# Optimization experiments

Measured on AMD Instinct MI355X. Metric: run time of the kernel, lower is better.

## Reference

```python
import jax, jax.numpy as jnp
import numpy as np

HIDDEN, N_HEADS, N_KV, HD = 2560, 32, 8, 80
B, S = 2, 2048

def apply_rope(x, cos_f, sin_f):
    # x: [B, S, H, hd]; cos_f/sin_f: [S, hd]
    seq_len = x.shape[1]
    cos = cos_f[:seq_len][None, :, None, :]
    sin = sin_f[:seq_len][None, :, None, :]
    hd = x.shape[-1]
    x1, x2 = x[..., : hd // 2], x[..., hd // 2 :]
    return x * cos + jnp.concatenate([-x2, x1], axis=-1) * sin


def setup_inputs() -> dict:
    key = jax.random.key(0)
    ks = jax.random.split(key, 7)
    sd = 0.02
    return {
        "x": jax.random.normal(ks[0], (B, S, HIDDEN), dtype=jnp.float32),
        "cos_f": jax.random.uniform(ks[1], (S, HD), dtype=jnp.float32),
        "sin_f": jax.random.uniform(ks[2], (S, HD), dtype=jnp.float32),
        "Wq": jax.random.normal(ks[3], (HIDDEN, N_HEADS * HD), dtype=jnp.float32) * sd,
        "Wk": jax.random.normal(ks[4], (HIDDEN, N_KV * HD), dtype=jnp.float32) * sd,
        "Wv": jax.random.normal(ks[5], (HIDDEN, N_KV * HD), dtype=jnp.float32) * sd,
        "Wo": jax.random.normal(ks[6], (N_HEADS * HD, HIDDEN), dtype=jnp.float32) * sd,
    }


def reference(x, cos_f, sin_f, Wq, Wk, Wv, Wo):
    b, s, _ = x.shape
    q = (x @ Wq).reshape(b, s, N_HEADS, HD)
    k = (x @ Wk).reshape(b, s, N_KV, HD)
    v = (x @ Wv).reshape(b, s, N_KV, HD)
    q = apply_rope(q, cos_f, sin_f)
    k = apply_rope(k, cos_f, sin_f)
    g = N_HEADS // N_KV
    k = jnp.repeat(k, g, axis=2)  # [b, s, n_heads, hd]
    v = jnp.repeat(v, g, axis=2)
    q, k, v = [jnp.transpose(t, (0, 2, 1, 3)) for t in (q, k, v)]  # [b, h, s, hd]
    scale = jnp.sqrt(jnp.float32(HD))
    w = jnp.einsum("bhqd,bhkd->bhqk", q, k) / scale
    causal = jnp.triu(jnp.full((s, s), -1e9, dtype=w.dtype), k=1)
    w = w + causal[None, None]
    w = jax.nn.softmax(w.astype(jnp.float32), axis=-1).astype(q.dtype)
    o = jnp.einsum("bhqk,bhkd->bhqd", w, v)
    o = jnp.transpose(o, (0, 2, 1, 3)).reshape(b, s, N_HEADS * HD)
    return o @ Wo
```

## Files before the change

kernel.cpp:

```cpp
#include <hip/hip_runtime.h>
#include <hip/hip_bf16.h>
#include <math.h>

#define HIDDEN 2560
#define NH 32
#define NKV 8
#define HD 80
#define BATCH 2
#define SEQ 2048
#define QH_COLS (NH*HD)
#define KV_COLS (NKV*HD)
#define QKV_COLS (QH_COLS + 2*KV_COLS)
#define ROWS (BATCH*SEQ)

typedef __attribute__((ext_vector_type(4))) float floatx4;
typedef __attribute__((ext_vector_type(16))) float floatx16;
typedef __attribute__((ext_vector_type(8))) short shortx8;
typedef __attribute__((ext_vector_type(4))) unsigned short u16x4;
typedef unsigned short u16;

__device__ inline u16 f2bf(float f) { __hip_bfloat16 h = __float2bfloat16(f); return *(u16*)&h; }
__device__ inline void storeC(float v, float* p) { *p = v; }
__device__ inline void storeC(float v, u16* p) { *p = f2bf(v); }

#if __has_builtin(__builtin_amdgcn_exp2f)
__device__ inline float fexp2(float x) { return __builtin_amdgcn_exp2f(x); }
#else
__device__ inline float fexp2(float x) { return __expf(x * 0.6931471805599453f); }
#endif

__device__ __forceinline__ unsigned cvtpk(float lo, float hi2) {
    unsigned r;
    asm("v_cvt_pk_bf16_f32 %0, %1, %2" : "=v"(r) : "v"(lo), "v"(hi2));
    return r;
}
__device__ __forceinline__ void pl32swap(unsigned &a, unsigned &b) {
#if __has_builtin(__builtin_amdgcn_permlane32_swap)
    auto r = __builtin_amdgcn_permlane32_swap(a, b, false, false);
    a = r[0]; b = r[1];
#else
    asm("v_permlane32_swap_b32 %0, %1" : "+v"(a), "+v"(b));
#endif
}

#define GLL(gp, lp) __builtin_amdgcn_global_load_lds( \
    (const __attribute__((address_space(1))) unsigned int*)(gp), \
    (__attribute__((address_space(3))) unsigned int*)(lp), 16, 0, 0)

__global__ __launch_bounds__(256) void conv_bf16(const float* __restrict__ x,
                                                 u16* __restrict__ y) {
    int i = (blockIdx.x * 256 + threadIdx.x) * 4;
    float4 v = *(const float4*)(x + i);
    u16x4 o = { f2bf(v.x), f2bf(v.y), f2bf(v.z), f2bf(v.w) };
    *(u16x4*)(y + i) = o;
}

__global__ __launch_bounds__(256) void transpose_conv(const float* __restrict__ W,
                                                      u16* __restrict__ Wt,
                                                      int K, int N) {
    __shared__ float tile[64][65];
    const int tid = threadIdx.x;
    const int n0 = blockIdx.x * 64, k0 = blockIdx.y * 64;
    const int r = tid >> 4, c4 = (tid & 15) * 4;
#pragma unroll
    for (int i = 0; i < 4; i++) {
        float4 v = *(const float4*)(W + (size_t)(k0 + r + i * 16) * N + n0 + c4);
        tile[r + i * 16][c4 + 0] = v.x;
        tile[r + i * 16][c4 + 1] = v.y;
        tile[r + i * 16][c4 + 2] = v.z;
        tile[r + i * 16][c4 + 3] = v.w;
    }
    __syncthreads();
    const int n = tid >> 2, kg = (tid & 3) * 16;
    __align__(16) u16 tmp[16];
#pragma unroll
    for (int j = 0; j < 16; j++) tmp[j] = f2bf(tile[kg + j][n]);
    u16* dst = Wt + (size_t)(n0 + n) * K + k0 + kg;
    *(uint4*)dst = *(const uint4*)tmp;
    *(uint4*)(dst + 8) = *(const uint4*)(tmp + 8);
}

template <typename OutT>
__global__ __launch_bounds__(512, 2) void gemm256(const u16* __restrict__ A,
                                                  const u16* __restrict__ Bt,
                                                  OutT* __restrict__ C,
                                                  int M, int N, int K) {
    __shared__ __align__(16) u16 SM[65536];
    const int tid = threadIdx.x;
    const int wave = tid >> 6, lane = tid & 63;
    const int m16 = lane & 15, quad = lane >> 4;
    const int wm = wave >> 2, wn = wave & 3;
    const int bm = blockIdx.y * 256, bn = blockIdx.x * 256;

    const int srow = (wave & 3) * 64 + lane;
    const int skc  = wave >> 2;
    const u16* pA = A  + (size_t)(bm + srow) * K + skc * 8;
    const u16* pB = Bt + (size_t)(bn + srow) * K + skc * 8;
    u16* lsA = SM + skc * 2048 + (wave & 3) * 512 + lane * 8;
    u16* lsB = lsA + 32768;

    const int aoff = quad * 2048 + (wm * 128 + m16) * 8;
    const int boff = quad * 2048 + (wn * 64 + m16) * 8 + 32768;

    floatx4 acc[8][4];
#pragma unroll
    for (int i = 0; i < 8; i++)
#pragma unroll
        for (int j = 0; j < 4; j++) acc[i][j] = (floatx4){0.f, 0.f, 0.f, 0.f};

    const int nkt = K >> 6;

#pragma unroll
    for (int t = 0; t < 2; t++) {
        const int tb = t * 16384, tc = t * 64;
        GLL(pA + tc,      lsA + tb);        GLL(pA + tc + 16, lsA + tb + 4096);
        GLL(pB + tc,      lsB + tb);        GLL(pB + tc + 16, lsB + tb + 4096);
        GLL(pA + tc + 32, lsA + tb + 8192); GLL(pA + tc + 48, lsA + tb + 12288);
        GLL(pB + tc + 32, lsB + tb + 8192); GLL(pB + tc + 48, lsB + tb + 12288);
    }
    asm volatile("s_waitcnt vmcnt(8)" ::: "memory");
    __builtin_amdgcn_s_barrier();

    for (int kt = 0; kt < nkt; ++kt) {
        const int ab = (kt & 1) * 16384;
        const bool pf = (kt + 2 < nkt);
        const int pc = (kt + 2) * 64;
        shortx8 af[8], b0, b1, b2, b3;

#pragma unroll
        for (int i = 0; i < 8; i++) af[i] = *(const shortx8*)(SM + ab + aoff + i * 128);
        b0 = *(const shortx8*)(SM + ab + boff);
        b1 = *(const shortx8*)(SM + ab + boff + 128);
        if (pf) { GLL(pA + pc, lsA + ab); GLL(pA + pc + 16, lsA + ab + 4096); }
        __builtin_amdgcn_s_barrier();
        __builtin_amdgcn_s_setprio(1);
#pragma unroll
        for (int i = 0; i < 8; i++) {
            acc[i][0] = __builtin_amdgcn_mfma_f32_16x16x32_bf16(af[i], b0, acc[i][0], 0, 0, 0);
            acc[i][1] = __builtin_amdgcn_mfma_f32_16x16x32_bf16(af[i], b1, acc[i][1], 0, 0, 0);
        }
        __builtin_amdgcn_s_setprio(0);
        __builtin_amdgcn_s_barrier();

        b2 = *(const shortx8*)(SM + ab + boff + 256);
        b3 = *(const shortx8*)(SM + ab + boff + 384);
        if (pf) { GLL(pB + pc, lsB + ab); GLL(pB + pc + 16, lsB + ab + 4096); }
        __builtin_amdgcn_s_barrier();
        __builtin_amdgcn_s_setprio(1);
#pragma unroll
        for (int i = 0; i < 8; i++) {
            acc[i][2] = __builtin_amdgcn_mfma_f32_16x16x32_bf16(af[i], b2, acc[i][2], 0, 0, 0);
            acc[i][3] = __builtin_amdgcn_mfma_f32_16x16x32_bf16(af[i], b3, acc[i][3], 0, 0, 0);
        }
        __builtin_amdgcn_s_setprio(0);
        __builtin_amdgcn_s_barrier();

#pragma unroll
        for (int i = 0; i < 8; i++) af[i] = *(const shortx8*)(SM + ab + 8192 + aoff + i * 128);
        b0 = *(const shortx8*)(SM + ab + 8192 + boff);
        b1 = *(const shortx8*)(SM + ab + 8192 + boff + 128);
        if (pf) { GLL(pA + pc + 32, lsA + ab + 8192); GLL(pA + pc + 48, lsA + ab + 12288); }
        __builtin_amdgcn_s_barrier();
        __builtin_amdgcn_s_setprio(1);
#pragma unroll
        for (int i = 0; i < 8; i++) {
            acc[i][0] = __builtin_amdgcn_mfma_f32_16x16x32_bf16(af[i], b0, acc[i][0], 0, 0, 0);
            acc[i][1] = __builtin_amdgcn_mfma_f32_16x16x32_bf16(af[i], b1, acc[i][1], 0, 0, 0);
        }
        __builtin_amdgcn_s_setprio(0);
        __builtin_amdgcn_s_barrier();

        b2 = *(const shortx8*)(SM + ab + 8192 + boff + 256);
        b3 = *(const shortx8*)(SM + ab + 8192 + boff + 384);
        if (pf) { GLL(pB + pc + 32, lsB + ab + 8192); GLL(pB + pc + 48, lsB + ab + 12288); }
        __builtin_amdgcn_s_barrier();
        __builtin_amdgcn_s_setprio(1);
#pragma unroll
        for (int i = 0; i < 8; i++) {
            acc[i][2] = __builtin_amdgcn_mfma_f32_16x16x32_bf16(af[i], b2, acc[i][2], 0, 0, 0);
            acc[i][3] = __builtin_amdgcn_mfma_f32_16x16x32_bf16(af[i], b3, acc[i][3], 0, 0, 0);
        }
        __builtin_amdgcn_s_setprio(0);
        if (pf) asm volatile("s_waitcnt vmcnt(8)" ::: "memory");
        else    asm volatile("s_waitcnt vmcnt(0)" ::: "memory");
        __builtin_amdgcn_s_barrier();
    }

#pragma unroll
    for (int i = 0; i < 8; i++)
#pragma unroll
        for (int j = 0; j < 4; j++)
#pragma unroll
            for (int p = 0; p < 4; p++) {
                int row = bm + wm * 128 + i * 16 + quad * 4 + p;
                int col = bn + wn * 64 + j * 16 + m16;
                storeC(acc[i][j][p], &C[(size_t)row * N + col]);
            }
}

__global__ __launch_bounds__(256) void rope_bf16(__hip_bfloat16* __restrict__ qkv,
                                                 const float* __restrict__ cf,
                                                 const float* __restrict__ sf) {
    int idx = blockIdx.x * 256 + threadIdx.x;
    int d  = idx % 40;
    int t  = idx / 40;
    int hh = t % (NH + NKV);
    int g  = t / (NH + NKV);
    int s  = g & (SEQ - 1);
    float c1 = cf[s * HD + d],      s1 = sf[s * HD + d];
    float c2 = cf[s * HD + d + 40], s2 = sf[s * HD + d + 40];
    const float qsc = (hh < NH) ? (float)(0.11180339887498949 * 1.4426950408889634) : 1.0f;
    __hip_bfloat16* p = (hh < NH) ? (qkv + (size_t)g * QKV_COLS + hh * HD)
                                  : (qkv + (size_t)g * QKV_COLS + QH_COLS + (hh - NH) * HD);
    float x1 = __bfloat162float(p[d]);
    float x2 = __bfloat162float(p[d + 40]);
    p[d]      = __float2bfloat16((x1 * c1 - x2 * s1) * qsc);
    p[d + 40] = __float2bfloat16((x2 * c2 + x1 * s2) * qsc);
}

__device__ __forceinline__ void stage_K(const u16* kg, u16* dst, int wave, int lane) {
#pragma unroll
    for (int t = 0; t < 2; t++) {
        int s = t * 256 + wave * 64 + lane;
        int db = t * 4 + wave;
        GLL(kg + (size_t)lane * QKV_COLS + db * 8, dst + s * 8);
    }
    if (wave < 2) {
        int s = 512 + wave * 64 + lane;
        int db = 8 + wave;
        GLL(kg + (size_t)lane * QKV_COLS + db * 8, dst + s * 8);
    }
}

__device__ __forceinline__ void load_V(const u16* vg, shortx8* vr, int wave, int lane) {
#pragma unroll
    for (int t = 0; t < 2; t++) {
        int db = t * 4 + wave;
        vr[t] = *(const shortx8*)(vg + (size_t)lane * QKV_COLS + db * 8);
    }
    if (wave < 2) vr[2] = *(const shortx8*)(vg + (size_t)lane * QKV_COLS + (8 + wave) * 8);
}

__device__ __forceinline__ void scatter_V(u16* Vs, const shortx8* vr, int wave, int lane) {
    const int kc = lane >> 3, jj = lane & 7;
    u16* base = Vs + kc * 768 + jj;
#pragma unroll
    for (int t = 0; t < 2; t++) {
        int db = t * 4 + wave;
#pragma unroll
        for (int i = 0; i < 8; i++) base[db * 64 + ((i ^ kc) << 3)] = vr[t][i];
    }
    if (wave < 2) {
        int db = 8 + wave;
#pragma unroll
        for (int i = 0; i < 8; i++) base[db * 64 + ((i ^ kc) << 3)] = vr[2][i];
    }
}

__global__ __launch_bounds__(256, 3) void attn_mfma(const u16* __restrict__ qkv,
                                                    u16* __restrict__ ob) {
    __shared__ __align__(16) u16 SM[16384];
    u16* Kbuf = SM;
    u16* Vs   = SM + 10240;

    const int tid  = threadIdx.x;
    const int wave = tid >> 6;
    const int lane = tid & 63;
    const int l31  = lane & 31;
    const int hi   = lane >> 5;

    const int idx = blockIdx.x;
    const int qt  = 15 - (idx >> 6);
    const int hb  = idx & 63;
    const int h   = hb >> 1;
    const int b   = hb & 1;
    const int kvh = h >> 2;
    const int qb  = qt * 128 + wave * 32;

    const u16* qgb = qkv + (size_t)(b * SEQ + qt * 128) * QKV_COLS + h * HD;
    const u16* kg0 = qkv + (size_t)(b * SEQ) * QKV_COLS + QH_COLS + kvh * HD;
    const u16* vg0 = qkv + (size_t)(b * SEQ) * QKV_COLS + QH_COLS + KV_COLS + kvh * HD;

    {
        int kc = tid >> 5, o = (tid & 31) * 4;
        *(u16x4*)(Vs + kc * 768 + 640 + o) = (u16x4){0, 0, 0, 0};
    }

#pragma unroll
    for (int t = 0; t < 5; t++) {
        int s = t * 256 + tid;
        int row = s / 10, ch = s % 10;
        GLL(qgb + (size_t)row * QKV_COLS + ch * 8, SM + s * 8);
    }
    __syncthreads();
    shortx8 qf[5];
    {
        const u16* qrow = SM + (wave * 32 + l31) * 80 + hi * 8;
#pragma unroll
        for (int c = 0; c < 5; c++) qf[c] = *(const shortx8*)(qrow + c * 16);
    }
    __syncthreads();

    int vbase[4];
#pragma unroll
    for (int c = 0; c < 4; c++) {
        int k8 = c * 2 + hi;
        vbase[c] = k8 * 768 + ((l31 & 24) + ((l31 & 7) ^ k8)) * 8;
    }
    const u16* kfp = Kbuf + hi * 512 + l31 * 8;

    stage_K(kg0, Kbuf, wave, lane);
    shortx8 vr[3];
    load_V(vg0, vr, wave, lane);
    __syncthreads();
    scatter_V(Vs, vr, wave, lane);
    __syncthreads();

    floatx16 Oacc[3];
#pragma unroll
    for (int n = 0; n < 3; n++)
#pragma unroll
        for (int r = 0; r < 16; r++) Oacc[n][r] = 0.0f;
    float mrow = -1.0e30f, lrow = 0.0f;
    int cur = 0;
    const int nkt = 2 * qt + 2;

    for (int kt = 0; kt < nkt; kt++) {
        const bool last = (kt == nkt - 1);
        if (!last) {
            const u16* kg = kg0 + (size_t)(kt + 1) * 64 * QKV_COLS;
            const u16* vg = vg0 + (size_t)(kt + 1) * 64 * QKV_COLS;
            stage_K(kg, Kbuf + (cur ^ 1) * 5120, wave, lane);
            load_V(vg, vr, wave, lane);
        }

        const bool active = (kt * 64 <= qb + 31);
        if (active) {
            const u16* kp = kfp + cur * 5120;
            const bool kr1   = (kt * 64 + 32 <= qb + 31);
            const bool dmask = (kt * 64 + 63 > qb);
            floatx16 S0, S1;
            {
                floatx16 s;
#pragma unroll
                for (int r = 0; r < 16; r++) s[r] = 0.0f;
#pragma unroll
                for (int c = 0; c < 5; c++) {
                    shortx8 kf = *(const shortx8*)(kp + c * 1024);
                    s = __builtin_amdgcn_mfma_f32_32x32x16_bf16(kf, qf[c], s, 0, 0, 0);
                }
                S0 = s;
            }
            if (kr1) {
                floatx16 s;
#pragma unroll
                for (int r = 0; r < 16; r++) s[r] = 0.0f;
#pragma unroll
                for (int c = 0; c < 5; c++) {
                    shortx8 kf = *(const shortx8*)(kp + c * 1024 + 256);
                    s = __builtin_amdgcn_mfma_f32_32x32x16_bf16(kf, qf[c], s, 0, 0, 0);
                }
                S1 = s;
            }
            const int qrel = qb + l31 - kt * 64;
            if (dmask) {
#pragma unroll
                for (int r = 0; r < 16; r++) {
                    int rr = (r & 3) + 8 * (r >> 2) + 4 * hi;
                    if (rr > qrel) S0[r] = -1.0e30f;
                    if (kr1 && (32 + rr) > qrel) S1[r] = -1.0e30f;
                }
            }
            float mx = mrow;
#pragma unroll
            for (int r = 0; r < 16; r++) mx = fmaxf(mx, S0[r]);
            if (kr1) {
#pragma unroll
                for (int r = 0; r < 16; r++) mx = fmaxf(mx, S1[r]);
            }
            mx = fmaxf(mx, __shfl_xor(mx, 32));
            if (!__all(mx - mrow <= 8.0f)) {
                float alpha = fexp2(mrow - mx);
                lrow *= alpha;
#pragma unroll
                for (int n = 0; n < 3; n++)
#pragma unroll
                    for (int r = 0; r < 16; r++) Oacc[n][r] *= alpha;
                mrow = mx;
            }
            float rsum = 0.0f;
#pragma unroll
            for (int r = 0; r < 16; r++) { float p = fexp2(S0[r] - mrow); rsum += p; S0[r] = p; }
            if (kr1) {
#pragma unroll
                for (int r = 0; r < 16; r++) { float p = fexp2(S1[r] - mrow); rsum += p; S1[r] = p; }
            }
            rsum += __shfl_xor(rsum, 32);
            lrow += rsum;

#pragma unroll
            for (int kr = 0; kr < 2; kr++) {
                if (kr == 1 && !kr1) break;
                floatx16& Sv = (kr == 0) ? S0 : S1;
                unsigned d0[4], d1[4];
#pragma unroll
                for (int m = 0; m < 4; m++) {
                    d0[m] = cvtpk(Sv[4 * m + 0], Sv[4 * m + 1]);
                    d1[m] = cvtpk(Sv[4 * m + 2], Sv[4 * m + 3]);
                }
#pragma unroll
                for (int cb = 0; cb < 2; cb++) {
                    int c = kr * 2 + cb;
                    if (kt * 64 + c * 16 > qb + 31) break;
                    unsigned x0 = d0[2 * cb], y0 = d0[2 * cb + 1];
                    unsigned x1 = d1[2 * cb], y1 = d1[2 * cb + 1];
                    pl32swap(x0, y0);
                    pl32swap(x1, y1);
                    union { unsigned u[4]; shortx8 s8; } pf;
                    pf.u[0] = x0; pf.u[1] = x1; pf.u[2] = y0; pf.u[3] = y1;
#pragma unroll
                    for (int n = 0; n < 3; n++) {
                        shortx8 vf = *(const shortx8*)(Vs + vbase[c] + n * 256);
                        Oacc[n] = __builtin_amdgcn_mfma_f32_32x32x16_bf16(vf, pf.s8, Oacc[n], 0, 0, 0);
                    }
                }
            }
        }

        if (last) break;
        __syncthreads();
        scatter_V(Vs, vr, wave, lane);
        cur ^= 1;
        __syncthreads();
    }

    const float invl = 1.0f / lrow;
    u16* op = ob + (size_t)(b * SEQ + qt * 128 + wave * 32 + l31) * QH_COLS + h * HD + 4 * hi;
#pragma unroll
    for (int n = 0; n < 3; n++) {
        const int mmax = (n == 2) ? 2 : 4;
#pragma unroll
        for (int m = 0; m < mmax; m++) {
            u16x4 o4 = { f2bf(Oacc[n][4 * m + 0] * invl), f2bf(Oacc[n][4 * m + 1] * invl),
                         f2bf(Oacc[n][4 * m + 2] * invl), f2bf(Oacc[n][4 * m + 3] * invl) };
            *(u16x4*)(op + n * 32 + 8 * m) = o4;
        }
    }
}

extern "C" void kernel_launch(void* const* d_in, const int* in_sizes, int n_in,
                              void* d_out, int out_size, void* d_ws, size_t ws_size,
                              hipStream_t stream) {
    const float* x    = (const float*)d_in[0];
    const float* cf   = (const float*)d_in[1];
    const float* sf   = (const float*)d_in[2];
    const float* Wq   = (const float*)d_in[3];
    const float* Wk   = (const float*)d_in[4];
    const float* Wv   = (const float*)d_in[5];
    const float* Wo   = (const float*)d_in[6];
    float* out = (float*)d_out;

    u16* xh    = (u16*)d_ws;
    u16* Wqkvt = xh    + (size_t)ROWS * HIDDEN;
    u16* Wot   = Wqkvt + (size_t)QKV_COLS * HIDDEN;
    u16* qkv   = Wot   + (size_t)QH_COLS * HIDDEN;
    u16* obh   = xh;

    dim3 blk(256);
    conv_bf16<<<(ROWS * HIDDEN / 4) / 256, blk, 0, stream>>>(x, xh);
    transpose_conv<<<dim3(QH_COLS / 64, HIDDEN / 64), blk, 0, stream>>>(Wq, Wqkvt, HIDDEN, QH_COLS);
    transpose_conv<<<dim3(KV_COLS / 64, HIDDEN / 64), blk, 0, stream>>>(Wk, Wqkvt + (size_t)QH_COLS * HIDDEN, HIDDEN, KV_COLS);
    transpose_conv<<<dim3(KV_COLS / 64, HIDDEN / 64), blk, 0, stream>>>(Wv, Wqkvt + (size_t)(QH_COLS + KV_COLS) * HIDDEN, HIDDEN, KV_COLS);
    transpose_conv<<<dim3(HIDDEN / 64, QH_COLS / 64), blk, 0, stream>>>(Wo, Wot, QH_COLS, HIDDEN);

    gemm256<u16><<<dim3(QKV_COLS / 256, ROWS / 256), dim3(512), 0, stream>>>(xh, Wqkvt, qkv, ROWS, QKV_COLS, HIDDEN);

    rope_bf16<<<(ROWS * (NH + NKV) * 40) / 256, blk, 0, stream>>>((__hip_bfloat16*)qkv, cf, sf);
    attn_mfma<<<dim3(16 * 64), blk, 0, stream>>>(qkv, obh);

    gemm256<float><<<dim3(HIDDEN / 256, ROWS / 256), dim3(512), 0, stream>>>(obh, Wot, out, ROWS, HIDDEN, QH_COLS);
}
```

Measured before the change: 479.9 us.

## Rewrite GEMM with 4-wave 32x32 MFMA tiles and XCD-aware block swizzle

```diff
diff --git a/kernel.cpp b/kernel.cpp
--- a/kernel.cpp
+++ b/kernel.cpp
@@ -81,121 +81,97 @@
 }
 
 template <typename OutT>
-__global__ __launch_bounds__(512, 2) void gemm256(const u16* __restrict__ A,
+__global__ __launch_bounds__(256, 1) void gemm256(const u16* __restrict__ A,
                                                   const u16* __restrict__ Bt,
                                                   OutT* __restrict__ C,
-                                                  int M, int N, int K) {
+                                                  int M, int N, int K,
+                                                  int nbx) {
     __shared__ __align__(16) u16 SM[65536];
     const int tid = threadIdx.x;
     const int wave = tid >> 6, lane = tid & 63;
-    const int m16 = lane & 15, quad = lane >> 4;
-    const int wm = wave >> 2, wn = wave & 3;
-    const int bm = blockIdx.y * 256, bn = blockIdx.x * 256;
-
-    const int srow = (wave & 3) * 64 + lane;
-    const int skc  = wave >> 2;
-    const u16* pA = A  + (size_t)(bm + srow) * K + skc * 8;
-    const u16* pB = Bt + (size_t)(bn + srow) * K + skc * 8;
-    u16* lsA = SM + skc * 2048 + (wave & 3) * 512 + lane * 8;
-    u16* lsB = lsA + 32768;
-
-    const int aoff = quad * 2048 + (wm * 128 + m16) * 8;
-    const int boff = quad * 2048 + (wn * 64 + m16) * 8 + 32768;
-
-    floatx4 acc[8][4];
-#pragma unroll
-    for (int i = 0; i < 8; i++)
-#pragma unroll
-        for (int j = 0; j < 4; j++) acc[i][j] = (floatx4){0.f, 0.f, 0.f, 0.f};
+    const int l31 = lane & 31, hi = lane >> 5;
+    const int wm = wave >> 1, wn = wave & 1;
+
+    const int nwg = nbx * (M >> 8);
+    const int cpx = nwg >> 3;
+    const int bid = (int)blockIdx.x;
+    const int swzb = (bid & 7) * cpx + (bid >> 3);
+    const int bm = (swzb / nbx) * 256, bn = (swzb % nbx) * 256;
+
+    const int srow = wave * 64 + lane;
+    const u16* gA = A  + (size_t)(bm + srow) * K;
+    const u16* gB = Bt + (size_t)(bn + srow) * K;
+    u16* lA = SM + srow * 8;
+    u16* lB = lA + 16384;
+
+    const int aoff = hi * 2048 + (wm * 128 + l31) * 8;
+    const int boff = hi * 2048 + (wn * 128 + l31) * 8 + 16384;
+
+    floatx16 acc[4][4];
+#pragma unroll
+    for (int m = 0; m < 4; m++)
+#pragma unroll
+        for (int n = 0; n < 4; n++)
+#pragma unroll
+            for (int r = 0; r < 16; r++) acc[m][n][r] = 0.0f;
 
     const int nkt = K >> 6;
 
 #pragma unroll
-    for (int t = 0; t < 2; t++) {
-        const int tb = t * 16384, tc = t * 64;
-        GLL(pA + tc,      lsA + tb);        GLL(pA + tc + 16, lsA + tb + 4096);
-        GLL(pB + tc,      lsB + tb);        GLL(pB + tc + 16, lsB + tb + 4096);
-        GLL(pA + tc + 32, lsA + tb + 8192); GLL(pA + tc + 48, lsA + tb + 12288);
-        GLL(pB + tc + 32, lsB + tb + 8192); GLL(pB + tc + 48, lsB + tb + 12288);
-    }
-    asm volatile("s_waitcnt vmcnt(8)" ::: "memory");
+    for (int kc = 0; kc < 8; kc++) {
+        GLL(gA + kc * 8,      lA + kc * 2048);
+        GLL(gB + kc * 8,      lB + kc * 2048);
+        GLL(gA + 64 + kc * 8, lA + 32768 + kc * 2048);
+        GLL(gB + 64 + kc * 8, lB + 32768 + kc * 2048);
+    }
+    asm volatile("s_waitcnt vmcnt(16)" ::: "memory");
     __builtin_amdgcn_s_barrier();
 
     for (int kt = 0; kt < nkt; ++kt) {
-        const int ab = (kt & 1) * 16384;
-        const bool pf = (kt + 2 < nkt);
-        const int pc = (kt + 2) * 64;
-        shortx8 af[8], b0, b1, b2, b3;
-
-#pragma unroll
-        for (int i = 0; i < 8; i++) af[i] = *(const shortx8*)(SM + ab + aoff + i * 128);
-        b0 = *(const shortx8*)(SM + ab + boff);
-        b1 = *(const shortx8*)(SM + ab + boff + 128);
-        if (pf) { GLL(pA + pc, lsA + ab); GLL(pA + pc + 16, lsA + ab + 4096); }
+        const int ab = (kt & 1) * 32768;
+#pragma unroll
+        for (int ks = 0; ks < 4; ks++) {
+            shortx8 a[4], b[4];
+#pragma unroll
+            for (int m = 0; m < 4; m++)
+                a[m] = *(const shortx8*)(SM + ab + ks * 4096 + aoff + m * 256);
+#pragma unroll
+            for (int n = 0; n < 4; n++)
+                b[n] = *(const shortx8*)(SM + ab + ks * 4096 + boff + n * 256);
+#pragma unroll
+            for (int m = 0; m < 4; m++)
+#pragma unroll
+                for (int n = 0; n < 4; n++)
+                    acc[m][n] = __builtin_amdgcn_mfma_f32_32x32x16_bf16(a[m], b[n], acc[m][n], 0, 0, 0);
+        }
+        if (kt == nkt - 1) break;
         __builtin_amdgcn_s_barrier();
-        __builtin_amdgcn_s_setprio(1);
-#pragma unroll
-        for (int i = 0; i < 8; i++) {
-            acc[i][0] = __builtin_amdgcn_mfma_f32_16x16x32_bf16(af[i], b0, acc[i][0], 0, 0, 0);
-            acc[i][1] = __builtin_amdgcn_mfma_f32_16x16x32_bf16(af[i], b1, acc[i][1], 0, 0, 0);
+        if (kt + 2 < nkt) {
+            const int pc = (kt + 2) * 64;
+#pragma unroll
+            for (int kc = 0; kc < 8; kc++) {
+                GLL(gA + pc + kc * 8, lA + ab + kc * 2048);
+                GLL(gB + pc + kc * 8, lB + ab + kc * 2048);
+            }
+            asm volatile("s_waitcnt vmcnt(16)" ::: "memory");
+        } else {
+            asm volatile("s_waitcnt vmcnt(0)" ::: "memory");
         }
-        __builtin_amdgcn_s_setprio(0);
         __builtin_amdgcn_s_barrier();
-
-        b2 = *(const shortx8*)(SM + ab + boff + 256);
-        b3 = *(const shortx8*)(SM + ab + boff + 384);
-        if (pf) { GLL(pB + pc, lsB + ab); GLL(pB + pc + 16, lsB + ab + 4096); }
-        __builtin_amdgcn_s_barrier();
-        __builtin_amdgcn_s_setprio(1);
-#pragma unroll
-        for (int i = 0; i < 8; i++) {
-            acc[i][2] = __builtin_amdgcn_mfma_f32_16x16x32_bf16(af[i], b2, acc[i][2], 0, 0, 0);
-            acc[i][3] = __builtin_amdgcn_mfma_f32_16x16x32_bf16(af[i], b3, acc[i][3], 0, 0, 0);
-        }
-        __builtin_amdgcn_s_setprio(0);
-        __builtin_amdgcn_s_barrier();
-
-#pragma unroll
-        for (int i = 0; i < 8; i++) af[i] = *(const shortx8*)(SM + ab + 8192 + aoff + i * 128);
-        b0 = *(const shortx8*)(SM + ab + 8192 + boff);
-        b1 = *(const shortx8*)(SM + ab + 8192 + boff + 128);
-        if (pf) { GLL(pA + pc + 32, lsA + ab + 8192); GLL(pA + pc + 48, lsA + ab + 12288); }
-        __builtin_amdgcn_s_barrier();
-        __builtin_amdgcn_s_setprio(1);
-#pragma unroll
-        for (int i = 0; i < 8; i++) {
-            acc[i][0] = __builtin_amdgcn_mfma_f32_16x16x32_bf16(af[i], b0, acc[i][0], 0, 0, 0);
-            acc[i][1] = __builtin_amdgcn_mfma_f32_16x16x32_bf16(af[i], b1, acc[i][1], 0, 0, 0);
-        }
-        __builtin_amdgcn_s_setprio(0);
-        __builtin_amdgcn_s_barrier();
-
-        b2 = *(const shortx8*)(SM + ab + 8192 + boff + 256);
-        b3 = *(const shortx8*)(SM + ab + 8192 + boff + 384);
-        if (pf) { GLL(pB + pc + 32, lsB + ab + 8192); GLL(pB + pc + 48, lsB + ab + 12288); }
-        __builtin_amdgcn_s_barrier();
-        __builtin_amdgcn_s_setprio(1);
-#pragma unroll
-        for (int i = 0; i < 8; i++) {
-            acc[i][2] = __builtin_amdgcn_mfma_f32_16x16x32_bf16(af[i], b2, acc[i][2], 0, 0, 0);
-            acc[i][3] = __builtin_amdgcn_mfma_f32_16x16x32_bf16(af[i], b3, acc[i][3], 0, 0, 0);
-        }
-        __builtin_amdgcn_s_setprio(0);
-        if (pf) asm volatile("s_waitcnt vmcnt(8)" ::: "memory");
-        else    asm volatile("s_waitcnt vmcnt(0)" ::: "memory");
-        __builtin_amdgcn_s_barrier();
-    }
-
-#pragma unroll
-    for (int i = 0; i < 8; i++)
-#pragma unroll
-        for (int j = 0; j < 4; j++)
-#pragma unroll
-            for (int p = 0; p < 4; p++) {
-                int row = bm + wm * 128 + i * 16 + quad * 4 + p;
-                int col = bn + wn * 64 + j * 16 + m16;
-                storeC(acc[i][j][p], &C[(size_t)row * N + col]);
-            }
+    }
+
+#pragma unroll
+    for (int m = 0; m < 4; m++)
+#pragma unroll
+        for (int n = 0; n < 4; n++)
+#pragma unroll
+            for (int g = 0; g < 4; g++)
+#pragma unroll
+                for (int p = 0; p < 4; p++) {
+                    int row = bm + wm * 128 + m * 32 + g * 8 + hi * 4 + p;
+                    int col = bn + wn * 128 + n * 32 + l31;
+                    storeC(acc[m][n][g * 4 + p], &C[(size_t)row * N + col]);
+                }
 }
 
 __global__ __launch_bounds__(256) void rope_bf16(__hip_bfloat16* __restrict__ qkv,
@@ -473,10 +449,10 @@
     transpose_conv<<<dim3(KV_COLS / 64, HIDDEN / 64), blk, 0, stream>>>(Wv, Wqkvt + (size_t)(QH_COLS + KV_COLS) * HIDDEN, HIDDEN, KV_COLS);
     transpose_conv<<<dim3(HIDDEN / 64, QH_COLS / 64), blk, 0, stream>>>(Wo, Wot, QH_COLS, HIDDEN);
 
-    gemm256<u16><<<dim3(QKV_COLS / 256, ROWS / 256), dim3(512), 0, stream>>>(xh, Wqkvt, qkv, ROWS, QKV_COLS, HIDDEN);
+    gemm256<u16><<<dim3((QKV_COLS / 256) * (ROWS / 256)), blk, 0, stream>>>(xh, Wqkvt, qkv, ROWS, QKV_COLS, HIDDEN, QKV_COLS / 256);
 
     rope_bf16<<<(ROWS * (NH + NKV) * 40) / 256, blk, 0, stream>>>((__hip_bfloat16*)qkv, cf, sf);
     attn_mfma<<<dim3(16 * 64), blk, 0, stream>>>(qkv, obh);
 
-    gemm256<float><<<dim3(HIDDEN / 256, ROWS / 256), dim3(512), 0, stream>>>(obh, Wot, out, ROWS, HIDDEN, QH_COLS);
-}
+    gemm256<float><<<dim3((HIDDEN / 256) * (ROWS / 256)), blk, 0, stream>>>(obh, Wot, out, ROWS, HIDDEN, QH_COLS, HIDDEN / 256);
+}
```

Result: slower. 644.3 us (+34.2%).

## Restructure GEMM pipeline into half-tile stages with XCD-aware block swizzle

Applied to the files above, without the earlier changes.

```diff
diff --git a/kernel.cpp b/kernel.cpp
--- a/kernel.cpp
+++ b/kernel.cpp
@@ -84,20 +84,26 @@
 __global__ __launch_bounds__(512, 2) void gemm256(const u16* __restrict__ A,
                                                   const u16* __restrict__ Bt,
                                                   OutT* __restrict__ C,
-                                                  int M, int N, int K) {
+                                                  int M, int N, int K,
+                                                  int nbx) {
     __shared__ __align__(16) u16 SM[65536];
     const int tid = threadIdx.x;
     const int wave = tid >> 6, lane = tid & 63;
     const int m16 = lane & 15, quad = lane >> 4;
     const int wm = wave >> 2, wn = wave & 3;
-    const int bm = blockIdx.y * 256, bn = blockIdx.x * 256;
+
+    const int nwg = nbx * (M >> 8);
+    const int cpx = nwg >> 3;
+    const int bid = (int)blockIdx.x;
+    const int swzb = (bid & 7) * cpx + (bid >> 3);
+    const int bm = (swzb / nbx) * 256, bn = (swzb % nbx) * 256;
 
     const int srow = (wave & 3) * 64 + lane;
-    const int skc  = wave >> 2;
-    const u16* pA = A  + (size_t)(bm + srow) * K + skc * 8;
-    const u16* pB = Bt + (size_t)(bn + srow) * K + skc * 8;
-    u16* lsA = SM + skc * 2048 + (wave & 3) * 512 + lane * 8;
-    u16* lsB = lsA + 32768;
+    const int kc0 = wave >> 2;
+    const u16* pA = A  + (size_t)(bm + srow) * K;
+    const u16* pB = Bt + (size_t)(bn + srow) * K;
+    u16* lA = SM + srow * 8;
+    u16* lB = lA + 32768;
 
     const int aoff = quad * 2048 + (wm * 128 + m16) * 8;
     const int boff = quad * 2048 + (wn * 64 + m16) * 8 + 32768;
@@ -111,78 +117,151 @@
     const int nkt = K >> 6;
 
 #pragma unroll
-    for (int t = 0; t < 2; t++) {
-        const int tb = t * 16384, tc = t * 64;
-        GLL(pA + tc,      lsA + tb);        GLL(pA + tc + 16, lsA + tb + 4096);
-        GLL(pB + tc,      lsB + tb);        GLL(pB + tc + 16, lsB + tb + 4096);
-        GLL(pA + tc + 32, lsA + tb + 8192); GLL(pA + tc + 48, lsA + tb + 12288);
-        GLL(pB + tc + 32, lsB + tb + 8192); GLL(pB + tc + 48, lsB + tb + 12288);
-    }
+    for (int g = 0; g < 2; g++) { int kc = kc0 + 2 * g;
+        GLL(pA + kc * 8, lA + kc * 2048); GLL(pB + kc * 8, lB + kc * 2048); }
+#pragma unroll
+    for (int g = 0; g < 2; g++) { int kc = 4 + kc0 + 2 * g;
+        GLL(pA + kc * 8, lA + kc * 2048); GLL(pB + kc * 8, lB + kc * 2048); }
+#pragma unroll
+    for (int g = 0; g < 2; g++) { int kc = kc0 + 2 * g;
+        GLL(pA + 64 + kc * 8, lA + 16384 + kc * 2048);
+        GLL(pB + 64 + kc * 8, lB + 16384 + kc * 2048); }
     asm volatile("s_waitcnt vmcnt(8)" ::: "memory");
     __builtin_amdgcn_s_barrier();
 
     for (int kt = 0; kt < nkt; ++kt) {
         const int ab = (kt & 1) * 16384;
-        const bool pf = (kt + 2 < nkt);
-        const int pc = (kt + 2) * 64;
-        shortx8 af[8], b0, b1, b2, b3;
-
-#pragma unroll
-        for (int i = 0; i < 8; i++) af[i] = *(const shortx8*)(SM + ab + aoff + i * 128);
-        b0 = *(const shortx8*)(SM + ab + boff);
-        b1 = *(const shortx8*)(SM + ab + boff + 128);
-        if (pf) { GLL(pA + pc, lsA + ab); GLL(pA + pc + 16, lsA + ab + 4096); }
+        const int pb = ab ^ 16384;
+
+        {
+            const u16* bp = SM + ab + boff;
+            const u16* ap = SM + ab + aoff;
+            shortx8 b0 = *(const shortx8*)(bp);
+            shortx8 b1 = *(const shortx8*)(bp + 128);
+            shortx8 b2 = *(const shortx8*)(bp + 256);
+            shortx8 b3 = *(const shortx8*)(bp + 384);
+            shortx8 a0 = *(const shortx8*)(ap);
+            shortx8 a1 = *(const shortx8*)(ap + 128);
+            shortx8 a2 = *(const shortx8*)(ap + 256);
+            shortx8 a3 = *(const shortx8*)(ap + 384);
+            if (kt + 1 < nkt) {
+                const int tc = (kt + 1) * 64;
+#pragma unroll
+                for (int g = 0; g < 2; g++) {
+                    int kc = 4 + kc0 + 2 * g;
+                    GLL(pA + tc + kc * 8, lA + pb + kc * 2048);
+                    GLL(pB + tc + kc * 8, lB + pb + kc * 2048);
+                }
+            }
+            __builtin_amdgcn_s_setprio(1);
+            acc[0][0] = __builtin_amdgcn_mfma_f32_16x16x32_bf16(a0, b0, acc[0][0], 0, 0, 0);
+            acc[0][1] = __builtin_amdgcn_mfma_f32_16x16x32_bf16(a0, b1, acc[0][1], 0, 0, 0);
+            acc[0][2] = __builtin_amdgcn_mfma_f32_16x16x32_bf16(a0, b2, acc[0][2], 0, 0, 0);
+            acc[0][3] = __builtin_amdgcn_mfma_f32_16x16x32_bf16(a0, b3, acc[0][3], 0, 0, 0);
+            acc[1][0] = __builtin_amdgcn_mfma_f32_16x16x32_bf16(a1, b0, acc[1][0], 0, 0, 0);
+            acc[1][1] = __builtin_amdgcn_mfma_f32_16x16x32_bf16(a1, b1, acc[1][1], 0, 0, 0);
+            acc[1][2] = __builtin_amdgcn_mfma_f32_16x16x32_bf16(a1, b2, acc[1][2], 0, 0, 0);
+            acc[1][3] = __builtin_amdgcn_mfma_f32_16x16x32_bf16(a1, b3, acc[1][3], 0, 0, 0);
+            acc[2][0] = __builtin_amdgcn_mfma_f32_16x16x32_bf16(a2, b0, acc[2][0], 0, 0, 0);
+            acc[2][1] = __builtin_amdgcn_mfma_f32_16x16x32_bf16(a2, b1, acc[2][1], 0, 0, 0);
+            acc[2][2] = __builtin_amdgcn_mfma_f32_16x16x32_bf16(a2, b2, acc[2][2], 0, 0, 0);
+            acc[2][3] = __builtin_amdgcn_mfma_f32_16x16x32_bf16(a2, b3, acc[2][3], 0, 0, 0);
+            acc[3][0] = __builtin_amdgcn_mfma_f32_16x16x32_bf16(a3, b0, acc[3][0], 0, 0, 0);
+            acc[3][1] = __builtin_amdgcn_mfma_f32_16x16x32_bf16(a3, b1, acc[3][1], 0, 0, 0);
+            acc[3][2] = __builtin_amdgcn_mfma_f32_16x16x32_bf16(a3, b2, acc[3][2], 0, 0, 0);
+            acc[3][3] = __builtin_amdgcn_mfma_f32_16x16x32_bf16(a3, b3, acc[3][3], 0, 0, 0);
+            __builtin_amdgcn_s_setprio(0);
+            a0 = *(const shortx8*)(ap + 512);
+            a1 = *(const shortx8*)(ap + 640);
+            a2 = *(const shortx8*)(ap + 768);
+            a3 = *(const shortx8*)(ap + 896);
+            __builtin_amdgcn_s_setprio(1);
+            acc[4][0] = __builtin_amdgcn_mfma_f32_16x16x32_bf16(a0, b0, acc[4][0], 0, 0, 0);
+            acc[4][1] = __builtin_amdgcn_mfma_f32_16x16x32_bf16(a0, b1, acc[4][1], 0, 0, 0);
+            acc[4][2] = __builtin_amdgcn_mfma_f32_16x16x32_bf16(a0, b2, acc[4][2], 0, 0, 0);
+            acc[4][3] = __builtin_amdgcn_mfma_f32_16x16x32_bf16(a0, b3, acc[4][3], 0, 0, 0);
+            acc[5][0] = __builtin_amdgcn_mfma_f32_16x16x32_bf16(a1, b0, acc[5][0], 0, 0, 0);
+            acc[5][1] = __builtin_amdgcn_mfma_f32_16x16x32_bf16(a1, b1, acc[5][1], 0, 0, 0);
+            acc[5][2] = __builtin_amdgcn_mfma_f32_16x16x32_bf16(a1, b2, acc[5][2], 0, 0, 0);
+            acc[5][3] = __builtin_amdgcn_mfma_f32_16x16x32_bf16(a1, b3, acc[5][3], 0, 0, 0);
+            acc[6][0] = __builtin_amdgcn_mfma_f32_16x16x32_bf16(a2, b0, acc[6][0], 0, 0, 0);
+            acc[6][1] = __builtin_amdgcn_mfma_f32_16x16x32_bf16(a2, b1, acc[6][1], 0, 0, 0);
+            acc[6][2] = __builtin_amdgcn_mfma_f32_16x16x32_bf16(a2, b2, acc[6][2], 0, 0, 0);
+            acc[6][3] = __builtin_amdgcn_mfma_f32_16x16x32_bf16(a2, b3, acc[6][3], 0, 0, 0);
+            acc[7][0] = __builtin_amdgcn_mfma_f32_16x16x32_bf16(a3, b0, acc[7][0], 0, 0, 0);
+            acc[7][1] = __builtin_amdgcn_mfma_f32_16x16x32_bf16(a3, b1, acc[7][1], 0, 0, 0);
+            acc[7][2] = __builtin_amdgcn_mfma_f32_16x16x32_bf16(a3, b2, acc[7][2], 0, 0, 0);
+            acc[7][3] = __builtin_amdgcn_mfma_f32_16x16x32_bf16(a3, b3, acc[7][3], 0, 0, 0);
+            __builtin_amdgcn_s_setprio(0);
+        }
+        if (kt + 1 < nkt) asm volatile("s_waitcnt vmcnt(8)" ::: "memory");
+        else              asm volatile("s_waitcnt vmcnt(0)" ::: "memory");
         __builtin_amdgcn_s_barrier();
-        __builtin_amdgcn_s_setprio(1);
-#pragma unroll
-        for (int i = 0; i < 8; i++) {
-            acc[i][0] = __builtin_amdgcn_mfma_f32_16x16x32_bf16(af[i], b0, acc[i][0], 0, 0, 0);
-            acc[i][1] = __builtin_amdgcn_mfma_f32_16x16x32_bf16(af[i], b1, acc[i][1], 0, 0, 0);
+
+        {
+            const u16* bp = SM + ab + 8192 + boff;
+            const u16* ap = SM + ab + 8192 + aoff;
+            shortx8 b0 = *(const shortx8*)(bp);
+            shortx8 b1 = *(const shortx8*)(bp + 128);
+            shortx8 b2 = *(const shortx8*)(bp + 256);
+            shortx8 b3 = *(const shortx8*)(bp + 384);
+            shortx8 a0 = *(const shortx8*)(ap);
+            shortx8 a1 = *(const shortx8*)(ap + 128);
+            shortx8 a2 = *(const shortx8*)(ap + 256);
+            shortx8 a3 = *(const shortx8*)(ap + 384);
+            if (kt + 2 < nkt) {
+                const int tc = (kt + 2) * 64;
+#pragma unroll
+                for (int g = 0; g < 2; g++) {
+                    int kc = kc0 + 2 * g;
+                    GLL(pA + tc + kc * 8, lA + ab + kc * 2048);
+                    GLL(pB + tc + kc * 8, lB + ab + kc * 2048);
+                }
+            }
+            __builtin_amdgcn_s_setprio(1);
+            acc[0][0] = __builtin_amdgcn_mfma_f32_16x16x32_bf16(a0, b0, acc[0][0], 0, 0, 0);
+            acc[0][1] = __builtin_amdgcn_mfma_f32_16x16x32_bf16(a0, b1, acc[0][1], 0, 0, 0);
+            acc[0][2] = __builtin_amdgcn_mfma_f32_16x16x32_bf16(a0, b2, acc[0][2], 0, 0, 0);
+            acc[0][3] = __builtin_amdgcn_mfma_f32_16x16x32_bf16(a0, b3, acc[0][3], 0, 0, 0);
+            acc[1][0] = __builtin_amdgcn_mfma_f32_16x16x32_bf16(a1, b0, acc[1][0], 0, 0, 0);
+            acc[1][1] = __builtin_amdgcn_mfma_f32_16x16x32_bf16(a1, b1, acc[1][1], 0, 0, 0);
+            acc[1][2] = __builtin_amdgcn_mfma_f32_16x16x32_bf16(a1, b2, acc[1][2], 0, 0, 0);
+            acc[1][3] = __builtin_amdgcn_mfma_f32_16x16x32_bf16(a1, b3, acc[1][3], 0, 0, 0);
+            acc[2][0] = __builtin_amdgcn_mfma_f32_16x16x32_bf16(a2, b0, acc[2][0], 0, 0, 0);
+            acc[2][1] = __builtin_amdgcn_mfma_f32_16x16x32_bf16(a2, b1, acc[2][1], 0, 0, 0);
+            acc[2][2] = __builtin_amdgcn_mfma_f32_16x16x32_bf16(a2, b2, acc[2][2], 0, 0, 0);
+            acc[2][3] = __builtin_amdgcn_mfma_f32_16x16x32_bf16(a2, b3, acc[2][3], 0, 0, 0);
+            acc[3][0] = __builtin_amdgcn_mfma_f32_16x16x32_bf16(a3, b0, acc[3][0], 0, 0, 0);
+            acc[3][1] = __builtin_amdgcn_mfma_f32_16x16x32_bf16(a3, b1, acc[3][1], 0, 0, 0);
+            acc[3][2] = __builtin_amdgcn_mfma_f32_16x16x32_bf16(a3, b2, acc[3][2], 0, 0, 0);
+            acc[3][3] = __builtin_amdgcn_mfma_f32_16x16x32_bf16(a3, b3, acc[3][3], 0, 0, 0);
+            __builtin_amdgcn_s_setprio(0);
+            a0 = *(const shortx8*)(ap + 512);
+            a1 = *(const shortx8*)(ap + 640);
+            a2 = *(const shortx8*)(ap + 768);
+            a3 = *(const shortx8*)(ap + 896);
+            __builtin_amdgcn_s_setprio(1);
+            acc[4][0] = __builtin_amdgcn_mfma_f32_16x16x32_bf16(a0, b0, acc[4][0], 0, 0, 0);
+            acc[4][1] = __builtin_amdgcn_mfma_f32_16x16x32_bf16(a0, b1, acc[4][1], 0, 0, 0);
+            acc[4][2] = __builtin_amdgcn_mfma_f32_16x16x32_bf16(a0, b2, acc[4][2], 0, 0, 0);
+            acc[4][3] = __builtin_amdgcn_mfma_f32_16x16x32_bf16(a0, b3, acc[4][3], 0, 0, 0);
+            acc[5][0] = __builtin_amdgcn_mfma_f32_16x16x32_bf16(a1, b0, acc[5][0], 0, 0, 0);
+            acc[5][1] = __builtin_amdgcn_mfma_f32_16x16x32_bf16(a1, b1, acc[5][1], 0, 0, 0);
+            acc[5][2] = __builtin_amdgcn_mfma_f32_16x16x32_bf16(a1, b2, acc[5][2], 0, 0, 0);
+            acc[5][3] = __builtin_amdgcn_mfma_f32_16x16x32_bf16(a1, b3, acc[5][3], 0, 0, 0);
+            acc[6][0] = __builtin_amdgcn_mfma_f32_16x16x32_bf16(a2, b0, acc[6][0], 0, 0, 0);
+            acc[6][1] = __builtin_amdgcn_mfma_f32_16x16x32_bf16(a2, b1, acc[6][1], 0, 0, 0);
+            acc[6][2] = __builtin_amdgcn_mfma_f32_16x16x32_bf16(a2, b2, acc[6][2], 0, 0, 0);
+            acc[6][3] = __builtin_amdgcn_mfma_f32_16x16x32_bf16(a2, b3, acc[6][3], 0, 0, 0);
+            acc[7][0] = __builtin_amdgcn_mfma_f32_16x16x32_bf16(a3, b0, acc[7][0], 0, 0, 0);
+            acc[7][1] = __builtin_amdgcn_mfma_f32_16x16x32_bf16(a3, b1, acc[7][1], 0, 0, 0);
+            acc[7][2] = __builtin_amdgcn_mfma_f32_16x16x32_bf16(a3, b2, acc[7][2], 0, 0, 0);
+            acc[7][3] = __builtin_amdgcn_mfma_f32_16x16x32_bf16(a3, b3, acc[7][3], 0, 0, 0);
+            __builtin_amdgcn_s_setprio(0);
         }
-        __builtin_amdgcn_s_setprio(0);
-        __builtin_amdgcn_s_barrier();
-
-        b2 = *(const shortx8*)(SM + ab + boff + 256);
-        b3 = *(const shortx8*)(SM + ab + boff + 384);
-        if (pf) { GLL(pB + pc, lsB + ab); GLL(pB + pc + 16, lsB + ab + 4096); }
-        __builtin_amdgcn_s_barrier();
-        __builtin_amdgcn_s_setprio(1);
-#pragma unroll
-        for (int i = 0; i < 8; i++) {
-            acc[i][2] = __builtin_amdgcn_mfma_f32_16x16x32_bf16(af[i], b2, acc[i][2], 0, 0, 0);
-            acc[i][3] = __builtin_amdgcn_mfma_f32_16x16x32_bf16(af[i], b3, acc[i][3], 0, 0, 0);
-        }
-        __builtin_amdgcn_s_setprio(0);
-        __builtin_amdgcn_s_barrier();
-
-#pragma unroll
-        for (int i = 0; i < 8; i++) af[i] = *(const shortx8*)(SM + ab + 8192 + aoff + i * 128);
-        b0 = *(const shortx8*)(SM + ab + 8192 + boff);
-        b1 = *(const shortx8*)(SM + ab + 8192 + boff + 128);
-        if (pf) { GLL(pA + pc + 32, lsA + ab + 8192); GLL(pA + pc + 48, lsA + ab + 12288); }
-        __builtin_amdgcn_s_barrier();
-        __builtin_amdgcn_s_setprio(1);
-#pragma unroll
-        for (int i = 0; i < 8; i++) {
-            acc[i][0] = __builtin_amdgcn_mfma_f32_16x16x32_bf16(af[i], b0, acc[i][0], 0, 0, 0);
-            acc[i][1] = __builtin_amdgcn_mfma_f32_16x16x32_bf16(af[i], b1, acc[i][1], 0, 0, 0);
-        }
-        __builtin_amdgcn_s_setprio(0);
-        __builtin_amdgcn_s_barrier();
-
-        b2 = *(const shortx8*)(SM + ab + 8192 + boff + 256);
-        b3 = *(const shortx8*)(SM + ab + 8192 + boff + 384);
-        if (pf) { GLL(pB + pc + 32, lsB + ab + 8192); GLL(pB + pc + 48, lsB + ab + 12288); }
-        __builtin_amdgcn_s_barrier();
-        __builtin_amdgcn_s_setprio(1);
-#pragma unroll
-        for (int i = 0; i < 8; i++) {
-            acc[i][2] = __builtin_amdgcn_mfma_f32_16x16x32_bf16(af[i], b2, acc[i][2], 0, 0, 0);
-            acc[i][3] = __builtin_amdgcn_mfma_f32_16x16x32_bf16(af[i], b3, acc[i][3], 0, 0, 0);
-        }
-        __builtin_amdgcn_s_setprio(0);
-        if (pf) asm volatile("s_waitcnt vmcnt(8)" ::: "memory");
-        else    asm volatile("s_waitcnt vmcnt(0)" ::: "memory");
+        if (kt == nkt - 1) break;
+        if (kt + 2 < nkt) asm volatile("s_waitcnt vmcnt(8)" ::: "memory");
+        else              asm volatile("s_waitcnt vmcnt(4)" ::: "memory");
         __builtin_amdgcn_s_barrier();
     }
 
@@ -473,10 +552,10 @@
     transpose_conv<<<dim3(KV_COLS / 64, HIDDEN / 64), blk, 0, stream>>>(Wv, Wqkvt + (size_t)(QH_COLS + KV_COLS) * HIDDEN, HIDDEN, KV_COLS);
     transpose_conv<<<dim3(HIDDEN / 64, QH_COLS / 64), blk, 0, stream>>>(Wo, Wot, QH_COLS, HIDDEN);
 
-    gemm256<u16><<<dim3(QKV_COLS / 256, ROWS / 256), dim3(512), 0, stream>>>(xh, Wqkvt, qkv, ROWS, QKV_COLS, HIDDEN);
+    gemm256<u16><<<dim3((QKV_COLS / 256) * (ROWS / 256)), dim3(512), 0, stream>>>(xh, Wqkvt, qkv, ROWS, QKV_COLS, HIDDEN, QKV_COLS / 256);
 
     rope_bf16<<<(ROWS * (NH + NKV) * 40) / 256, blk, 0, stream>>>((__hip_bfloat16*)qkv, cf, sf);
     attn_mfma<<<dim3(16 * 64), blk, 0, stream>>>(qkv, obh);
 
-    gemm256<float><<<dim3(HIDDEN / 256, ROWS / 256), dim3(512), 0, stream>>>(obh, Wot, out, ROWS, HIDDEN, QH_COLS);
-}
+    gemm256<float><<<dim3((HIDDEN / 256) * (ROWS / 256)), dim3(512), 0, stream>>>(obh, Wot, out, ROWS, HIDDEN, QH_COLS, HIDDEN / 256);
+}
```

After: 547.8 us. 1.14x slower.
